# Performance work log

Measured on AMD Instinct MI355X. Metric: run time of the kernel, lower is better.

## Reference

```python
import jax, jax.numpy as jnp
import numpy as np

IN_CAPS, IN_SIZE = 2401, 8
OUT_CAPS, OUT_SIZE = 8, 16
ROUTING_ITERS = 3


def squash(s, axis):
    mag_sq = jnp.sum(s * s, axis=axis, keepdims=True)
    mag = jnp.sqrt(mag_sq)
    return mag_sq / (1.0 + mag_sq) * (s / mag)


def setup_inputs() -> dict:
    key = jax.random.key(0)
    kx, kw = jax.random.split(key)
    B = 256
    x = jax.random.normal(kx, (B, IN_CAPS, IN_SIZE), dtype=jnp.float32)
    stdv = 1.0 / np.sqrt(IN_CAPS)
    W = jax.random.uniform(kw, (IN_CAPS, OUT_CAPS, OUT_SIZE, IN_SIZE),
                           dtype=jnp.float32, minval=-stdv, maxval=stdv)
    return {"x": x, "W": W}


def reference(x, W):
    # u_hat[b,i,o,c] = W[i,o,c,d] @ x[b,i,d]   -> [B, 2401, 8, 16]
    u_hat = jnp.einsum('iocd,bid->bioc', W, x)
    u_hat_det = jax.lax.stop_gradient(u_hat)

    b_ij = jnp.zeros((IN_CAPS, OUT_CAPS), dtype=x.dtype)
    v_j = None
    for it in range(ROUTING_ITERS):
        c_ij = jax.nn.softmax(b_ij, axis=1)  # softmax over out_capsules
        last = (it == ROUTING_ITERS - 1)
        u = u_hat if last else u_hat_det
        s_j = jnp.einsum('io,bioc->boc', c_ij, u)  # [B, 8, 16]
        v_j = squash(s_j, axis=-1)
        if not last:
            # agreement: mean over batch of <u_hat_i, v_j>
            a = jnp.einsum('bioc,boc->io', u_hat_det, v_j) / x.shape[0]
            b_ij = b_ij + a
    return v_j  # [B, 8, 16]
```

## Files before the change

kernel.cpp:

```cpp
#include <hip/hip_runtime.h>
#include <math.h>

#define IC    2401
#define BSZ   256
#define OC    8
#define CS    16
#define OCC   128
#define XROW  19208
#define KP    19264
#define KTILES 301

typedef __attribute__((ext_vector_type(8))) short short8;
typedef __attribute__((ext_vector_type(4))) float f32x4;

__device__ __forceinline__ unsigned short f2bf(float f) {
    union { float f; unsigned u; } v; v.f = f;
    const unsigned r = v.u + 0x7FFF + ((v.u >> 16) & 1);
    return (unsigned short)(r >> 16);
}

__global__ __launch_bounds__(256)
void cvt_kernel(const float* __restrict__ x, unsigned short* __restrict__ xT)
{
    __shared__ float Ts[64 * 65];
    const int tid = threadIdx.x;
    const int bg  = blockIdx.x;
    const int kt  = blockIdx.y;
#pragma unroll
    for (int r = 0; r < 4; ++r) {
        const int flat = r * 256 + tid;
        const int b = flat >> 4, cq = flat & 15;
        const int col = kt * 64 + cq * 4;
        float4 v = make_float4(0.f, 0.f, 0.f, 0.f);
        if (col < XROW) v = *(const float4*)(x + (size_t)(bg * 64 + b) * XROW + col);
        *(float4*)&Ts[b * 65 + cq * 4] = v;
    }
    __syncthreads();
#pragma unroll
    for (int r = 0; r < 2; ++r) {
        const int flat = r * 256 + tid;
        const int rl = flat >> 3, bq = flat & 7;
        union { short8 v; unsigned short h[8]; } o;
#pragma unroll
        for (int j = 0; j < 8; ++j) o.h[j] = f2bf(Ts[(bq * 8 + j) * 65 + rl]);
        *(short8*)(xT + (size_t)(kt * 64 + rl) * 256 + bg * 64 + bq * 8) = o.v;
    }
}

__global__ __launch_bounds__(256)
void prep0_kernel(const float* __restrict__ W, unsigned short* __restrict__ cwt)
{
    __shared__ float Ws[8 * 1032];
    const int tid = threadIdx.x;
    const int i0  = blockIdx.x * 8;
#pragma unroll
    for (int r = 0; r < 8; ++r) {
        const int flat = r * 256 + tid;
        const int g = flat >> 8, rem = flat & 255;
        int gi = i0 + g; if (gi > 2400) gi = 2400;
        const float4 v = *(const float4*)(W + (size_t)gi * 1024 + rem * 4);
        *(float4*)&Ws[g * 1032 + rem * 4] = v;
    }
    __syncthreads();
#pragma unroll
    for (int r = 0; r < 4; ++r) {
        const int flat = r * 256 + tid;
        const int oc = flat >> 3, g = flat & 7;
        const int gi = i0 + g;
        union { short8 v; unsigned short h[8]; } o;
        if (gi <= 2400) {
            const float* wp = &Ws[g * 1032 + oc * 8];
#pragma unroll
            for (int j = 0; j < 8; ++j) o.h[j] = f2bf(0.125f * wp[j]);
        } else {
#pragma unroll
            for (int j = 0; j < 8; ++j) o.h[j] = 0;
        }
        *(short8*)(cwt + (size_t)oc * KP + (size_t)gi * 8) = o.v;
    }
}

__global__ __launch_bounds__(256, 4)
void s_gemm(const float* __restrict__ x, const unsigned short* __restrict__ cwt,
            float* __restrict__ spart)
{
    __shared__ __align__(16) unsigned short Xs[64 * 64];
    __shared__ __align__(16) unsigned short Bs[128 * 64];
    const int tid = threadIdx.x;
    const int bg  = blockIdx.x, iy = blockIdx.y, ni = gridDim.y;
    const int b0  = bg * 64;
    const int ln  = tid & 63;
    const int m0  = (tid >> 6) * 16;
    const int mr  = ln & 15, qd = ln >> 4;

    f32x4 acc[8];
#pragma unroll
    for (int n = 0; n < 8; ++n) acc[n] = (f32x4){0.f, 0.f, 0.f, 0.f};

    for (int kt = iy; kt < KTILES; kt += ni) {
        __syncthreads();
#pragma unroll
        for (int r = 0; r < 2; ++r) {
            const int flat = r * 256 + tid;
            const int b = flat >> 3, col = flat & 7;
            int gq = kt * 8 + col; if (gq > 2400) gq = 2400;
            const float4* xp = (const float4*)(x + (size_t)(b0 + b) * XROW + (size_t)gq * 8);
            const float4 u0 = xp[0], u1 = xp[1];
            union { short8 v; unsigned short h[8]; } o;
            o.h[0] = f2bf(u0.x); o.h[1] = f2bf(u0.y); o.h[2] = f2bf(u0.z); o.h[3] = f2bf(u0.w);
            o.h[4] = f2bf(u1.x); o.h[5] = f2bf(u1.y); o.h[6] = f2bf(u1.z); o.h[7] = f2bf(u1.w);
            *(short8*)&Xs[b * 64 + ((col ^ (b & 7)) * 8)] = o.v;
        }
#pragma unroll
        for (int r = 0; r < 4; ++r) {
            const int flat = r * 256 + tid;
            const int oc = flat >> 3, col = flat & 7;
            const short8 w = *(const short8*)(cwt + (size_t)oc * KP + (size_t)(kt * 8 + col) * 8);
            *(short8*)&Bs[oc * 64 + ((col ^ (oc & 7)) * 8)] = w;
        }
        __syncthreads();
#pragma unroll
        for (int kk = 0; kk < 2; ++kk) {
            const int csw = ((kk * 4 + qd) ^ (mr & 7)) * 8;
            const short8 a = *(const short8*)&Xs[(m0 + mr) * 64 + csw];
#pragma unroll
            for (int nt = 0; nt < 8; ++nt) {
                const short8 b = *(const short8*)&Bs[(nt * 16 + mr) * 64 + csw];
                acc[nt] = __builtin_amdgcn_mfma_f32_16x16x32_bf16(a, b, acc[nt], 0, 0, 0);
            }
        }
    }

    float* op = spart + ((size_t)iy * BSZ + b0) * OCC;
#pragma unroll
    for (int nt = 0; nt < 8; ++nt)
#pragma unroll
        for (int r = 0; r < 4; ++r)
            op[(size_t)(m0 + qd * 4 + r) * OCC + nt * 16 + mr] = acc[nt][r];
}

__global__ __launch_bounds__(256)
void squash_kernel(const float* __restrict__ spart, float* __restrict__ vout,
                   unsigned short* __restrict__ vT, int ni, int writeT)
{
    __shared__ float red[256 * 17];
    const int tid = threadIdx.x;
    const int r   = tid & 63;
    const int kq  = tid >> 6;
    const int row = blockIdx.x * 64 + r;

    float s[CS];
#pragma unroll
    for (int j = 0; j < CS; ++j) s[j] = 0.0f;
    for (int k = kq; k < ni; k += 4) {
        const float4* p = (const float4*)(spart + (size_t)k * BSZ * OCC + (size_t)row * CS);
#pragma unroll
        for (int q = 0; q < 4; ++q) {
            const float4 t = p[q];
            s[4 * q + 0] += t.x; s[4 * q + 1] += t.y;
            s[4 * q + 2] += t.z; s[4 * q + 3] += t.w;
        }
    }
#pragma unroll
    for (int j = 0; j < CS; ++j) red[tid * 17 + j] = s[j];
    __syncthreads();
    if (tid < 64) {
#pragma unroll
        for (int j = 0; j < CS; ++j)
            s[j] = red[r * 17 + j] + red[(64 + r) * 17 + j]
                 + red[(128 + r) * 17 + j] + red[(192 + r) * 17 + j];
        float ms = 0.0f;
#pragma unroll
        for (int j = 0; j < CS; ++j) ms = fmaf(s[j], s[j], ms);
        const float scale = sqrtf(ms) / (1.0f + ms);
        if (writeT) {
            const int b = row >> 3, o = row & 7;
#pragma unroll
            for (int j = 0; j < CS; ++j)
                vT[(size_t)(o * 16 + j) * 256 + b] = f2bf(s[j] * scale);
        } else {
            float4* o4 = (float4*)(vout + (size_t)row * CS);
#pragma unroll
            for (int q = 0; q < 4; ++q)
                o4[q] = make_float4(s[4 * q + 0] * scale, s[4 * q + 1] * scale,
                                    s[4 * q + 2] * scale, s[4 * q + 3] * scale);
        }
    }
}

template<bool FIRST>
__global__ __launch_bounds__(256, 2)
void a_gemm(const unsigned short* __restrict__ xT, const unsigned short* __restrict__ vT,
            const float* __restrict__ W, float* __restrict__ bij,
            unsigned short* __restrict__ cwt)
{
    __shared__ __align__(16) char smraw[128 * 68 * 4];
    unsigned short* As = (unsigned short*)smraw;
    unsigned short* Bx = (unsigned short*)(smraw + 16384);
    float* Hs = (float*)smraw;

    const int tid = threadIdx.x;
    const int i0  = blockIdx.x * 8;
    const int ln  = tid & 63, wv = tid >> 6;
    const int mr  = ln & 15, qd = ln >> 4;

    f32x4 acc[2][4];
#pragma unroll
    for (int a = 0; a < 2; ++a)
#pragma unroll
        for (int b = 0; b < 4; ++b) acc[a][b] = (f32x4){0.f, 0.f, 0.f, 0.f};

    for (int bc = 0; bc < 4; ++bc) {
        __syncthreads();
#pragma unroll
        for (int r = 0; r < 4; ++r) {
            const int flat = r * 256 + tid;
            const int oc = flat >> 3, col = flat & 7;
            const short8 v = *(const short8*)(vT + (size_t)oc * 256 + bc * 64 + col * 8);
            *(short8*)&As[oc * 64 + ((col ^ (oc & 7)) * 8)] = v;
        }
#pragma unroll
        for (int r = 0; r < 2; ++r) {
            const int flat = r * 256 + tid;
            const int rw = flat >> 3, col = flat & 7;
            const short8 v = *(const short8*)(xT + (size_t)(i0 * 8 + rw) * 256 + bc * 64 + col * 8);
            *(short8*)&Bx[rw * 64 + ((col ^ (rw & 7)) * 8)] = v;
        }
        __syncthreads();
#pragma unroll
        for (int kk = 0; kk < 2; ++kk) {
            const int csw = ((kk * 4 + qd) ^ (mr & 7)) * 8;
#pragma unroll
            for (int nt = 0; nt < 4; ++nt) {
                const short8 b = *(const short8*)&Bx[(nt * 16 + mr) * 64 + csw];
#pragma unroll
                for (int mt = 0; mt < 2; ++mt) {
                    const short8 a = *(const short8*)&As[((wv * 2 + mt) * 16 + mr) * 64 + csw];
                    acc[mt][nt] = __builtin_amdgcn_mfma_f32_16x16x32_bf16(a, b, acc[mt][nt], 0, 0, 0);
                }
            }
        }
    }

    __syncthreads();
#pragma unroll
    for (int mt = 0; mt < 2; ++mt)
#pragma unroll
        for (int nt = 0; nt < 4; ++nt)
#pragma unroll
            for (int r = 0; r < 4; ++r)
                Hs[((wv * 2 + mt) * 16 + qd * 4 + r) * 68 + nt * 16 + mr] = acc[mt][nt][r];
    __syncthreads();

    const int ch = tid & 3, oo = (tid >> 2) & 7, il = tid >> 5;
    const int ival = i0 + il;
    const int gi = (ival < IC) ? ival : IC - 1;
    const float* Wt = W + (size_t)gi * 1024 + oo * 128 + ch * 32;

    float wreg[4][8];
#pragma unroll
    for (int c = 0; c < 4; ++c) {
        const float4 w0 = *(const float4*)(Wt + c * 8);
        const float4 w1 = *(const float4*)(Wt + c * 8 + 4);
        wreg[c][0] = w0.x; wreg[c][1] = w0.y; wreg[c][2] = w0.z; wreg[c][3] = w0.w;
        wreg[c][4] = w1.x; wreg[c][5] = w1.y; wreg[c][6] = w1.z; wreg[c][7] = w1.w;
    }
    float p = 0.0f;
#pragma unroll
    for (int c = 0; c < 4; ++c) {
        const float* hr = &Hs[(oo * 16 + ch * 4 + c) * 68 + il * 8];
        const float4 h0 = *(const float4*)hr;
        const float4 h1 = *(const float4*)(hr + 4);
        p = fmaf(wreg[c][0], h0.x, p); p = fmaf(wreg[c][1], h0.y, p);
        p = fmaf(wreg[c][2], h0.z, p); p = fmaf(wreg[c][3], h0.w, p);
        p = fmaf(wreg[c][4], h1.x, p); p = fmaf(wreg[c][5], h1.y, p);
        p = fmaf(wreg[c][6], h1.z, p); p = fmaf(wreg[c][7], h1.w, p);
    }
    p += __shfl_xor(p, 1); p += __shfl_xor(p, 2);
    const float anew = p * (1.0f / 256.0f);
    float bv = anew;
    if (!FIRST) bv += bij[gi * 8 + oo];
    float mx = bv;
    mx = fmaxf(mx, __shfl_xor(mx, 4));
    mx = fmaxf(mx, __shfl_xor(mx, 8));
    mx = fmaxf(mx, __shfl_xor(mx, 16));
    const float e = expf(bv - mx);
    float ss = e;
    ss += __shfl_xor(ss, 4); ss += __shfl_xor(ss, 8); ss += __shfl_xor(ss, 16);
    float cv = e / ss;
    if (ival >= IC) cv = 0.0f;
    if (ch == 0 && ival < IC) bij[ival * 8 + oo] = bv;
#pragma unroll
    for (int c = 0; c < 4; ++c) {
        union { short8 v; unsigned short h[8]; } o;
#pragma unroll
        for (int j = 0; j < 8; ++j) o.h[j] = f2bf(cv * wreg[c][j]);
        *(short8*)(cwt + (size_t)(oo * 16 + ch * 4 + c) * KP + (size_t)ival * 8) = o.v;
    }
}

extern "C" void kernel_launch(void* const* d_in, const int* in_sizes, int n_in,
                              void* d_out, int out_size, void* d_ws, size_t ws_size,
                              hipStream_t stream)
{
    const float* x = (const float*)d_in[0];
    const float* W = (const float*)d_in[1];
    float* out = (float*)d_out;

    const size_t xT_b  = (size_t)KP * 256 * 2;
    const size_t cwt_b = (size_t)128 * KP * 2;
    const size_t vT_b  = 128 * 256 * 2;
    const size_t bij_b = IC * 8 * 4;
    const size_t fixed = xT_b + cwt_b + vT_b + bij_b;

    int ni = 128;
    while (ni > 4 && (size_t)ni * BSZ * OCC * 4 + fixed > ws_size) ni >>= 1;

    char* p = (char*)d_ws;
    float*          spart = (float*)p;          p += (size_t)ni * BSZ * OCC * 4;
    unsigned short* xT    = (unsigned short*)p; p += xT_b;
    unsigned short* cwt   = (unsigned short*)p; p += cwt_b;
    unsigned short* vT    = (unsigned short*)p; p += vT_b;
    float*          bij   = (float*)p;

    const dim3 sgrid(4, ni);

    cvt_kernel<<<dim3(4, KTILES), 256, 0, stream>>>(x, xT);
    prep0_kernel<<<KTILES, 256, 0, stream>>>(W, cwt);

    s_gemm<<<sgrid, 256, 0, stream>>>(x, cwt, spart);
    squash_kernel<<<32, 256, 0, stream>>>(spart, nullptr, vT, ni, 1);
    a_gemm<true><<<KTILES, 256, 0, stream>>>(xT, vT, W, bij, cwt);
    s_gemm<<<sgrid, 256, 0, stream>>>(x, cwt, spart);
    squash_kernel<<<32, 256, 0, stream>>>(spart, nullptr, vT, ni, 1);
    a_gemm<false><<<KTILES, 256, 0, stream>>>(xT, vT, W, bij, cwt);
    s_gemm<<<sgrid, 256, 0, stream>>>(x, cwt, spart);
    squash_kernel<<<32, 256, 0, stream>>>(spart, out, vT, ni, 0);
}
```

Baseline: 162.0 us.

## Pre-convert x and W to bf16 once, merge prep kernels, retile s_gemm

Merges the two prep kernels into one launch that also writes a row-major bf16 copy of x and a bf16 copy of W. s_gemm now streams bf16 x instead of re-reading and converting fp32 x on every routing iteration, and a_gemm reads bf16 W, which halves that traffic. s_gemm gets a 2x4 warp tile with a fixed split count of 64 instead of a size chosen from workspace, and squash uses a wider grid with a shuffle reduction. This adds workspace and gives up the fallback when workspace is small, and W in a_gemm loses precision by going through bf16.

New measurement: 144.0 us. 1.12x faster.

```diff
diff --git a/kernel.cpp b/kernel.cpp
--- a/kernel.cpp
+++ b/kernel.cpp
@@ -1,14 +1,15 @@
 #include <hip/hip_runtime.h>
 #include <math.h>
 
-#define IC    2401
-#define BSZ   256
-#define OC    8
-#define CS    16
-#define OCC   128
-#define XROW  19208
-#define KP    19264
+#define IC     2401
+#define BSZ    256
+#define OC     8
+#define CS     16
+#define OCC    128
+#define XROW   19208
+#define KP     19264
 #define KTILES 301
+#define NI     64
 
 typedef __attribute__((ext_vector_type(8))) short short8;
 typedef __attribute__((ext_vector_type(4))) float f32x4;
@@ -18,98 +19,112 @@
     const unsigned r = v.u + 0x7FFF + ((v.u >> 16) & 1);
     return (unsigned short)(r >> 16);
 }
+__device__ __forceinline__ float bf2f(unsigned short h) {
+    union { unsigned u; float f; } v; v.u = ((unsigned)h) << 16;
+    return v.f;
+}
 
 __global__ __launch_bounds__(256)
-void cvt_kernel(const float* __restrict__ x, unsigned short* __restrict__ xT)
-{
-    __shared__ float Ts[64 * 65];
+void prep_kernel(const float* __restrict__ x, const float* __restrict__ W,
+                 unsigned short* __restrict__ xT, unsigned short* __restrict__ xB,
+                 unsigned short* __restrict__ Wbf, unsigned short* __restrict__ cwt)
+{
     const int tid = threadIdx.x;
-    const int bg  = blockIdx.x;
-    const int kt  = blockIdx.y;
-#pragma unroll
-    for (int r = 0; r < 4; ++r) {
-        const int flat = r * 256 + tid;
-        const int b = flat >> 4, cq = flat & 15;
-        const int col = kt * 64 + cq * 4;
-        float4 v = make_float4(0.f, 0.f, 0.f, 0.f);
-        if (col < XROW) v = *(const float4*)(x + (size_t)(bg * 64 + b) * XROW + col);
-        *(float4*)&Ts[b * 65 + cq * 4] = v;
-    }
-    __syncthreads();
-#pragma unroll
-    for (int r = 0; r < 2; ++r) {
-        const int flat = r * 256 + tid;
-        const int rl = flat >> 3, bq = flat & 7;
-        union { short8 v; unsigned short h[8]; } o;
-#pragma unroll
-        for (int j = 0; j < 8; ++j) o.h[j] = f2bf(Ts[(bq * 8 + j) * 65 + rl]);
-        *(short8*)(xT + (size_t)(kt * 64 + rl) * 256 + bg * 64 + bq * 8) = o.v;
-    }
-}
-
-__global__ __launch_bounds__(256)
-void prep0_kernel(const float* __restrict__ W, unsigned short* __restrict__ cwt)
-{
-    __shared__ float Ws[8 * 1032];
-    const int tid = threadIdx.x;
-    const int i0  = blockIdx.x * 8;
-#pragma unroll
-    for (int r = 0; r < 8; ++r) {
-        const int flat = r * 256 + tid;
-        const int g = flat >> 8, rem = flat & 255;
-        int gi = i0 + g; if (gi > 2400) gi = 2400;
-        const float4 v = *(const float4*)(W + (size_t)gi * 1024 + rem * 4);
-        *(float4*)&Ws[g * 1032 + rem * 4] = v;
-    }
-    __syncthreads();
-#pragma unroll
-    for (int r = 0; r < 4; ++r) {
-        const int flat = r * 256 + tid;
-        const int oc = flat >> 3, g = flat & 7;
-        const int gi = i0 + g;
-        union { short8 v; unsigned short h[8]; } o;
-        if (gi <= 2400) {
-            const float* wp = &Ws[g * 1032 + oc * 8];
-#pragma unroll
-            for (int j = 0; j < 8; ++j) o.h[j] = f2bf(0.125f * wp[j]);
-        } else {
-#pragma unroll
-            for (int j = 0; j < 8; ++j) o.h[j] = 0;
-        }
-        *(short8*)(cwt + (size_t)oc * KP + (size_t)gi * 8) = o.v;
-    }
-}
-
-__global__ __launch_bounds__(256, 4)
-void s_gemm(const float* __restrict__ x, const unsigned short* __restrict__ cwt,
+    if (blockIdx.x < 1204) {
+        __shared__ float Ts[64 * 65];
+        const int bg = blockIdx.x & 3;
+        const int kt = blockIdx.x >> 2;
+#pragma unroll
+        for (int r = 0; r < 4; ++r) {
+            const int flat = r * 256 + tid;
+            const int b = flat >> 4, cq = flat & 15;
+            const int col = kt * 64 + cq * 4;
+            float4 v = make_float4(0.f, 0.f, 0.f, 0.f);
+            if (col < XROW) v = *(const float4*)(x + (size_t)(bg * 64 + b) * XROW + col);
+            *(float4*)&Ts[b * 65 + cq * 4] = v;
+        }
+        __syncthreads();
+#pragma unroll
+        for (int r = 0; r < 2; ++r) {
+            const int flat = r * 256 + tid;
+            const int rl = flat >> 3, bq = flat & 7;
+            union { short8 v; unsigned short h[8]; } o;
+#pragma unroll
+            for (int j = 0; j < 8; ++j) o.h[j] = f2bf(Ts[(bq * 8 + j) * 65 + rl]);
+            *(short8*)(xT + (size_t)(kt * 64 + rl) * 256 + bg * 64 + bq * 8) = o.v;
+        }
+#pragma unroll
+        for (int r = 0; r < 2; ++r) {
+            const int flat = r * 256 + tid;
+            const int b = flat >> 3, g = flat & 7;
+            union { short8 v; unsigned short h[8]; } o;
+#pragma unroll
+            for (int j = 0; j < 8; ++j) o.h[j] = f2bf(Ts[b * 65 + g * 8 + j]);
+            *(short8*)(xB + (size_t)(bg * 64 + b) * KP + (size_t)kt * 64 + g * 8) = o.v;
+        }
+    } else {
+        __shared__ float Ws[8 * 1032];
+        const int i0 = (blockIdx.x - 1204) * 8;
+#pragma unroll
+        for (int r = 0; r < 8; ++r) {
+            const int flat = r * 256 + tid;
+            const int g = flat >> 8, rem = flat & 255;
+            int gi = i0 + g; if (gi > 2400) gi = 2400;
+            const float4 v = *(const float4*)(W + (size_t)gi * 1024 + rem * 4);
+            *(float4*)&Ws[g * 1032 + rem * 4] = v;
+        }
+        __syncthreads();
+#pragma unroll
+        for (int r = 0; r < 4; ++r) {
+            const int flat = r * 256 + tid;
+            const int oc = flat >> 3, g = flat & 7;
+            const int gi = i0 + g;
+            union { short8 v; unsigned short h[8]; } w, c;
+            if (gi <= 2400) {
+                const float* wp = &Ws[g * 1032 + oc * 8];
+#pragma unroll
+                for (int j = 0; j < 8; ++j) {
+                    w.h[j] = f2bf(wp[j]);
+                    c.h[j] = f2bf(0.125f * wp[j]);
+                }
+            } else {
+#pragma unroll
+                for (int j = 0; j < 8; ++j) { w.h[j] = 0; c.h[j] = 0; }
+            }
+            *(short8*)(Wbf + (size_t)oc * KP + (size_t)gi * 8) = w.v;
+            *(short8*)(cwt + (size_t)oc * KP + (size_t)gi * 8) = c.v;
+        }
+    }
+}
+
+__global__ __launch_bounds__(256, 2)
+void s_gemm(const unsigned short* __restrict__ xB, const unsigned short* __restrict__ cwt,
             float* __restrict__ spart)
 {
     __shared__ __align__(16) unsigned short Xs[64 * 64];
     __shared__ __align__(16) unsigned short Bs[128 * 64];
     const int tid = threadIdx.x;
-    const int bg  = blockIdx.x, iy = blockIdx.y, ni = gridDim.y;
+    const int bg  = blockIdx.x, iy = blockIdx.y;
     const int b0  = bg * 64;
     const int ln  = tid & 63;
-    const int m0  = (tid >> 6) * 16;
     const int mr  = ln & 15, qd = ln >> 4;
-
-    f32x4 acc[8];
-#pragma unroll
-    for (int n = 0; n < 8; ++n) acc[n] = (f32x4){0.f, 0.f, 0.f, 0.f};
-
-    for (int kt = iy; kt < KTILES; kt += ni) {
+    const int mh  = (tid >> 6) & 1;
+    const int nh  = tid >> 7;
+
+    f32x4 acc[2][4];
+#pragma unroll
+    for (int a = 0; a < 2; ++a)
+#pragma unroll
+        for (int b = 0; b < 4; ++b) acc[a][b] = (f32x4){0.f, 0.f, 0.f, 0.f};
+
+    for (int kt = iy; kt < KTILES; kt += NI) {
         __syncthreads();
 #pragma unroll
         for (int r = 0; r < 2; ++r) {
             const int flat = r * 256 + tid;
             const int b = flat >> 3, col = flat & 7;
-            int gq = kt * 8 + col; if (gq > 2400) gq = 2400;
-            const float4* xp = (const float4*)(x + (size_t)(b0 + b) * XROW + (size_t)gq * 8);
-            const float4 u0 = xp[0], u1 = xp[1];
-            union { short8 v; unsigned short h[8]; } o;
-            o.h[0] = f2bf(u0.x); o.h[1] = f2bf(u0.y); o.h[2] = f2bf(u0.z); o.h[3] = f2bf(u0.w);
-            o.h[4] = f2bf(u1.x); o.h[5] = f2bf(u1.y); o.h[6] = f2bf(u1.z); o.h[7] = f2bf(u1.w);
-            *(short8*)&Xs[b * 64 + ((col ^ (b & 7)) * 8)] = o.v;
+            const short8 v = *(const short8*)(xB + (size_t)(b0 + b) * KP + (size_t)(kt * 8 + col) * 8);
+            *(short8*)&Xs[b * 64 + ((col ^ (b & 7)) * 8)] = v;
         }
 #pragma unroll
         for (int r = 0; r < 4; ++r) {
@@ -122,68 +137,58 @@
 #pragma unroll
         for (int kk = 0; kk < 2; ++kk) {
             const int csw = ((kk * 4 + qd) ^ (mr & 7)) * 8;
-            const short8 a = *(const short8*)&Xs[(m0 + mr) * 64 + csw];
-#pragma unroll
-            for (int nt = 0; nt < 8; ++nt) {
-                const short8 b = *(const short8*)&Bs[(nt * 16 + mr) * 64 + csw];
-                acc[nt] = __builtin_amdgcn_mfma_f32_16x16x32_bf16(a, b, acc[nt], 0, 0, 0);
+            const short8 a0 = *(const short8*)&Xs[(mh * 32 + mr) * 64 + csw];
+            const short8 a1 = *(const short8*)&Xs[(mh * 32 + 16 + mr) * 64 + csw];
+#pragma unroll
+            for (int nt = 0; nt < 4; ++nt) {
+                const short8 b = *(const short8*)&Bs[(nh * 64 + nt * 16 + mr) * 64 + csw];
+                acc[0][nt] = __builtin_amdgcn_mfma_f32_16x16x32_bf16(a0, b, acc[0][nt], 0, 0, 0);
+                acc[1][nt] = __builtin_amdgcn_mfma_f32_16x16x32_bf16(a1, b, acc[1][nt], 0, 0, 0);
             }
         }
     }
 
     float* op = spart + ((size_t)iy * BSZ + b0) * OCC;
 #pragma unroll
-    for (int nt = 0; nt < 8; ++nt)
-#pragma unroll
-        for (int r = 0; r < 4; ++r)
-            op[(size_t)(m0 + qd * 4 + r) * OCC + nt * 16 + mr] = acc[nt][r];
+    for (int mt = 0; mt < 2; ++mt)
+#pragma unroll
+        for (int nt = 0; nt < 4; ++nt)
+#pragma unroll
+            for (int r = 0; r < 4; ++r)
+                op[(size_t)(mh * 32 + mt * 16 + qd * 4 + r) * OCC + nh * 64 + nt * 16 + mr]
+                    = acc[mt][nt][r];
 }
 
 __global__ __launch_bounds__(256)
 void squash_kernel(const float* __restrict__ spart, float* __restrict__ vout,
-                   unsigned short* __restrict__ vT, int ni, int writeT)
-{
-    __shared__ float red[256 * 17];
+                   unsigned short* __restrict__ vT, int writeT)
+{
+    __shared__ float red[256];
     const int tid = threadIdx.x;
-    const int r   = tid & 63;
-    const int kq  = tid >> 6;
-    const int row = blockIdx.x * 64 + r;
-
-    float s[CS];
-#pragma unroll
-    for (int j = 0; j < CS; ++j) s[j] = 0.0f;
-    for (int k = kq; k < ni; k += 4) {
-        const float4* p = (const float4*)(spart + (size_t)k * BSZ * OCC + (size_t)row * CS);
-#pragma unroll
-        for (int q = 0; q < 4; ++q) {
-            const float4 t = p[q];
-            s[4 * q + 0] += t.x; s[4 * q + 1] += t.y;
-            s[4 * q + 2] += t.z; s[4 * q + 3] += t.w;
-        }
-    }
-#pragma unroll
-    for (int j = 0; j < CS; ++j) red[tid * 17 + j] = s[j];
+    const int r0  = blockIdx.x * 8;
+    const int idx = tid & 127;
+    const int k0  = tid >> 7;
+
+    const float* base = spart + (size_t)r0 * 16 + idx;
+    float acc = 0.0f;
+#pragma unroll 8
+    for (int k = k0; k < NI; k += 2) acc += base[(size_t)k * (BSZ * OCC)];
+    red[tid] = acc;
     __syncthreads();
-    if (tid < 64) {
-#pragma unroll
-        for (int j = 0; j < CS; ++j)
-            s[j] = red[r * 17 + j] + red[(64 + r) * 17 + j]
-                 + red[(128 + r) * 17 + j] + red[(192 + r) * 17 + j];
-        float ms = 0.0f;
-#pragma unroll
-        for (int j = 0; j < CS; ++j) ms = fmaf(s[j], s[j], ms);
+
+    if (tid < 128) {
+        const float s = red[tid] + red[tid + 128];
+        float ms = s * s;
+        ms += __shfl_xor(ms, 1); ms += __shfl_xor(ms, 2);
+        ms += __shfl_xor(ms, 4); ms += __shfl_xor(ms, 8);
         const float scale = sqrtf(ms) / (1.0f + ms);
+        const float outv = s * scale;
+        const int row = r0 + (tid >> 4);
+        const int j   = tid & 15;
         if (writeT) {
-            const int b = row >> 3, o = row & 7;
-#pragma unroll
-            for (int j = 0; j < CS; ++j)
-                vT[(size_t)(o * 16 + j) * 256 + b] = f2bf(s[j] * scale);
+            vT[(size_t)((row & 7) * 16 + j) * 256 + (row >> 3)] = f2bf(outv);
         } else {
-            float4* o4 = (float4*)(vout + (size_t)row * CS);
-#pragma unroll
-            for (int q = 0; q < 4; ++q)
-                o4[q] = make_float4(s[4 * q + 0] * scale, s[4 * q + 1] * scale,
-                                    s[4 * q + 2] * scale, s[4 * q + 3] * scale);
+            vout[(size_t)row * 16 + j] = outv;
         }
     }
 }
@@ -191,7 +196,7 @@
 template<bool FIRST>
 __global__ __launch_bounds__(256, 2)
 void a_gemm(const unsigned short* __restrict__ xT, const unsigned short* __restrict__ vT,
-            const float* __restrict__ W, float* __restrict__ bij,
+            const unsigned short* __restrict__ Wbf, float* __restrict__ bij,
             unsigned short* __restrict__ cwt)
 {
     __shared__ __align__(16) char smraw[128 * 68 * 4];
@@ -255,15 +260,15 @@
     const int ch = tid & 3, oo = (tid >> 2) & 7, il = tid >> 5;
     const int ival = i0 + il;
     const int gi = (ival < IC) ? ival : IC - 1;
-    const float* Wt = W + (size_t)gi * 1024 + oo * 128 + ch * 32;
+    const unsigned short* Wt = Wbf + (size_t)(oo * 16 + ch * 4) * KP + (size_t)gi * 8;
 
     float wreg[4][8];
 #pragma unroll
     for (int c = 0; c < 4; ++c) {
-        const float4 w0 = *(const float4*)(Wt + c * 8);
-        const float4 w1 = *(const float4*)(Wt + c * 8 + 4);
-        wreg[c][0] = w0.x; wreg[c][1] = w0.y; wreg[c][2] = w0.z; wreg[c][3] = w0.w;
-        wreg[c][4] = w1.x; wreg[c][5] = w1.y; wreg[c][6] = w1.z; wreg[c][7] = w1.w;
+        union { short8 v; unsigned short h[8]; } uw;
+        uw.v = *(const short8*)(Wt + (size_t)c * KP);
+#pragma unroll
+        for (int j = 0; j < 8; ++j) wreg[c][j] = bf2f(uw.h[j]);
     }
     float p = 0.0f;
 #pragma unroll
@@ -307,33 +312,25 @@
     const float* W = (const float*)d_in[1];
     float* out = (float*)d_out;
 
-    const size_t xT_b  = (size_t)KP * 256 * 2;
-    const size_t cwt_b = (size_t)128 * KP * 2;
-    const size_t vT_b  = 128 * 256 * 2;
-    const size_t bij_b = IC * 8 * 4;
-    const size_t fixed = xT_b + cwt_b + vT_b + bij_b;
-
-    int ni = 128;
-    while (ni > 4 && (size_t)ni * BSZ * OCC * 4 + fixed > ws_size) ni >>= 1;
-
     char* p = (char*)d_ws;
-    float*          spart = (float*)p;          p += (size_t)ni * BSZ * OCC * 4;
-    unsigned short* xT    = (unsigned short*)p; p += xT_b;
-    unsigned short* cwt   = (unsigned short*)p; p += cwt_b;
-    unsigned short* vT    = (unsigned short*)p; p += vT_b;
+    float*          spart = (float*)p;          p += (size_t)NI * BSZ * OCC * 4;
+    unsigned short* xT    = (unsigned short*)p; p += (size_t)KP * 256 * 2;
+    unsigned short* xB    = (unsigned short*)p; p += (size_t)256 * KP * 2;
+    unsigned short* Wbf   = (unsigned short*)p; p += (size_t)128 * KP * 2;
+    unsigned short* cwt   = (unsigned short*)p; p += (size_t)128 * KP * 2;
+    unsigned short* vT    = (unsigned short*)p; p += (size_t)128 * 256 * 2;
     float*          bij   = (float*)p;
 
-    const dim3 sgrid(4, ni);
-
-    cvt_kernel<<<dim3(4, KTILES), 256, 0, stream>>>(x, xT);
-    prep0_kernel<<<KTILES, 256, 0, stream>>>(W, cwt);
-
-    s_gemm<<<sgrid, 256, 0, stream>>>(x, cwt, spart);
-    squash_kernel<<<32, 256, 0, stream>>>(spart, nullptr, vT, ni, 1);
-    a_gemm<true><<<KTILES, 256, 0, stream>>>(xT, vT, W, bij, cwt);
-    s_gemm<<<sgrid, 256, 0, stream>>>(x, cwt, spart);
-    squash_kernel<<<32, 256, 0, stream>>>(spart, nullptr, vT, ni, 1);
-    a_gemm<false><<<KTILES, 256, 0, stream>>>(xT, vT, W, bij, cwt);
-    s_gemm<<<sgrid, 256, 0, stream>>>(x, cwt, spart);
-    squash_kernel<<<32, 256, 0, stream>>>(spart, out, vT, ni, 0);
-}
+    const dim3 sgrid(4, NI);
+
+    prep_kernel<<<1505, 256, 0, stream>>>(x, W, xT, xB, Wbf, cwt);
+
+    s_gemm<<<sgrid, 256, 0, stream>>>(xB, cwt, spart);
+    squash_kernel<<<256, 256, 0, stream>>>(spart, nullptr, vT, 1);
+    a_gemm<true><<<KTILES, 256, 0, stream>>>(xT, vT, Wbf, bij, cwt);
+    s_gemm<<<sgrid, 256, 0, stream>>>(xB, cwt, spart);
+    squash_kernel<<<256, 256, 0, stream>>>(spart, nullptr, vT, 1);
+    a_gemm<false><<<KTILES, 256, 0, stream>>>(xT, vT, Wbf, bij, cwt);
+    s_gemm<<<sgrid, 256, 0, stream>>>(xB, cwt, spart);
+    squash_kernel<<<256, 256, 0, stream>>>(spart, out, vT, 0);
+}
```
